# Kernel optimization log

Measured on AMD Instinct MI355X. Metric: run time of the kernel, lower is better.

## Reference

```python
import jax, jax.numpy as jnp
import numpy as np

# Dimensions
N = 16384    # batch of tree nodes (original code is batch-1 per node; math is identical per row)
WD, TD, RD = 300, 50, 50   # word / tag / rel feature dims
H = 512      # mlp_com_hid_dim
M = 512      # mem_dim == mlp_com_out_dim (required by additive gate combination)
G = 5        # gates: [i, f_down, f_left, o, u]
W_SCALE = 0.05


def setup_inputs() -> dict:
    key = jax.random.key(0)
    ks = jax.random.split(key, 32)
    def rn(i, shape, s=1.0):
        return jax.random.normal(ks[i], shape, dtype=jnp.float32) * s
    return dict(
        word=rn(0, (N, WD)), tag=rn(1, (N, TD)), rel=rn(2, (N, RD)),
        k=rn(3, (N, M)), q=rn(4, (N, M)), h_prev=rn(5, (N, M)), c_prev=rn(6, (N, M)),
        # com_MLP params, stacked over the 5 gates
        W_word=rn(7, (G, H, WD), W_SCALE), b_word=rn(8, (G, H), W_SCALE),
        W_tag=rn(9, (G, H, TD), W_SCALE),  b_tag=rn(10, (G, H), W_SCALE),
        W_rel=rn(11, (G, H, RD), W_SCALE), b_rel=rn(12, (G, H), W_SCALE),
        W_hid=rn(13, (G, H, H), W_SCALE),  b_hid=rn(14, (G, H), W_SCALE),
        W_last=rn(15, (G, M, H), W_SCALE), b_last=rn(16, (G, M), W_SCALE),
        # per-gate Linear(mem_dim, mem_dim) applied to h_prev and k
        W_hp=rn(17, (G, M, M), W_SCALE), b_hp=rn(18, (G, M), W_SCALE),
        W_k=rn(19, (G, M, M), W_SCALE),  b_k=rn(20, (G, M), W_SCALE),
    )


def reference(word, tag, rel, k, q, h_prev, c_prev,
              W_word, b_word, W_tag, b_tag, W_rel, b_rel,
              W_hid, b_hid, W_last, b_last,
              W_hp, b_hp, W_k, b_k):
    # com_MLP for all 5 gates at once (eval mode: dropout = identity)
    h0 = jnp.tanh(jnp.einsum('nw,ghw->gnh', word, W_word)
                  + jnp.einsum('nt,ght->gnh', tag, W_tag)
                  + jnp.einsum('nr,ghr->gnh', rel, W_rel)
                  + (b_word + b_tag + b_rel)[:, None, :])            # [G,N,H]
    h1 = jnp.tanh(jnp.einsum('gnh,gkh->gnk', h0, W_hid) + b_hid[:, None, :])   # hidden layer
    m = jnp.tanh(jnp.einsum('gnh,gmh->gnm', h1, W_last) + b_last[:, None, :])  # [G,N,M]
    # gate pre-activations: mlp + W_h h_prev + W_k k (with biases)
    pre = (m
           + jnp.einsum('nm,gom->gno', h_prev, W_hp) + b_hp[:, None, :]
           + jnp.einsum('nm,gom->gno', k, W_k) + b_k[:, None, :])    # [G,N,M]
    i_g    = jax.nn.sigmoid(pre[0])
    f_down = jax.nn.sigmoid(pre[1])
    f_left = jax.nn.sigmoid(pre[2])
    o_g    = jax.nn.sigmoid(pre[3])
    u_g    = jnp.tanh(pre[4])
    c = i_g * u_g + f_down * q + f_left * c_prev
    h = o_g * jnp.tanh(c)
    return (h, c)
```

## Files before the change

kernel.cpp:

```cpp
#include <hip/hip_runtime.h>
#include <math.h>

#define NROWS 16384
#define GATES 5
#define HDIM 512
#define KPAD 416

using bf16x8 = __attribute__((ext_vector_type(8))) short;
using f32x4  = __attribute__((ext_vector_type(4))) float;

__device__ inline float b2f(unsigned short s) {
  unsigned int u = ((unsigned int)s) << 16;
  return __builtin_bit_cast(float, u);
}
__device__ inline unsigned short f2b(float f) {
  unsigned int u = __builtin_bit_cast(unsigned int, f);
  u += 0x7fffu + ((u >> 16) & 1u);
  return (unsigned short)(u >> 16);
}

__device__ inline float fast_sigmoid(float x) {
  float t = __builtin_amdgcn_exp2f(-1.4426950408889634f * x);
  return __builtin_amdgcn_rcpf(1.0f + t);
}
__device__ inline float fast_tanh(float x) {
  float t = __builtin_amdgcn_exp2f(2.8853900817779268f * x);
  return 1.0f - 2.0f * __builtin_amdgcn_rcpf(1.0f + t);
}

__device__ inline void gload_lds16(const unsigned short* g, unsigned short* l) {
  __builtin_amdgcn_global_load_lds(
      (const __attribute__((address_space(1))) unsigned int*)(g),
      (__attribute__((address_space(3))) unsigned int*)(l), 16, 0, 0);
}


__global__ void pack_x(const float* __restrict__ word,
                       const float* __restrict__ tag,
                       const float* __restrict__ rel,
                       unsigned short* __restrict__ xcat) {
  int idx = blockIdx.x * 256 + threadIdx.x;
  if (idx >= NROWS * KPAD) return;
  int n = idx / KPAD, c = idx % KPAD;
  float v = 0.f;
  if (c < 300)      v = word[n * 300 + c];
  else if (c < 350) v = tag[n * 50 + (c - 300)];
  else if (c < 400) v = rel[n * 50 + (c - 350)];
  xcat[idx] = f2b(v);
}

__global__ void pack_w(const float* __restrict__ Ww,
                       const float* __restrict__ Wt,
                       const float* __restrict__ Wr,
                       unsigned short* __restrict__ Wcat) {
  int idx = blockIdx.x * 256 + threadIdx.x;
  if (idx >= GATES * HDIM * KPAD) return;
  int gh = idx / KPAD;
  int c = idx % KPAD;
  float v = 0.f;
  if (c < 300)      v = Ww[gh * 300 + c];
  else if (c < 350) v = Wt[gh * 50 + (c - 300)];
  else if (c < 400) v = Wr[gh * 50 + (c - 350)];
  Wcat[idx] = f2b(v);
}

__global__ void cvt_w4(const float* __restrict__ a, const float* __restrict__ b,
                       const float* __restrict__ c, const float* __restrict__ d,
                       unsigned short* oa, unsigned short* ob,
                       unsigned short* oc, unsigned short* od) {
  const float* in; unsigned short* out;
  switch (blockIdx.y) {
    case 0: in = a; out = oa; break;
    case 1: in = b; out = ob; break;
    case 2: in = c; out = oc; break;
    default: in = d; out = od; break;
  }
  int i = (blockIdx.x * 256 + threadIdx.x) * 4;
  float4 v = *(const float4*)(in + i);
  ushort4 o;
  o.x = f2b(v.x); o.y = f2b(v.y); o.z = f2b(v.z); o.w = f2b(v.w);
  *(ushort4*)(out + i) = o;
}

__global__ void cvt_x2(const float* __restrict__ a, const float* __restrict__ b,
                       unsigned short* oa, unsigned short* ob) {
  const float* in = blockIdx.y ? b : a;
  unsigned short* out = blockIdx.y ? ob : oa;
  int i = (blockIdx.x * 256 + threadIdx.x) * 4;
  float4 v = *(const float4*)(in + i);
  ushort4 o;
  o.x = f2b(v.x); o.y = f2b(v.y); o.z = f2b(v.z); o.w = f2b(v.w);
  *(ushort4*)(out + i) = o;
}

__global__ void pack_bias(const float* __restrict__ bw, const float* __restrict__ bt,
                          const float* __restrict__ br, const float* __restrict__ bh,
                          const float* __restrict__ bl, const float* __restrict__ bhp,
                          const float* __restrict__ bk,
                          float* bias0, float* bias1, float* bias2, float* biasD) {
  int i = blockIdx.x * 256 + threadIdx.x;
  if (i < GATES * HDIM) {
    bias0[i] = bw[i] + bt[i] + br[i];
    bias1[i] = bh[i];
    bias2[i] = bl[i];
    biasD[i] = bhp[i] + bk[i];
  }
}


template<int MODE>
__global__ __launch_bounds__(512, 2) void gemm_big(
    const unsigned short* __restrict__ A1, const unsigned short* __restrict__ A2,
    const unsigned short* __restrict__ W1, const unsigned short* __restrict__ W2,
    const float* __restrict__ bias,
    const unsigned short* __restrict__ Madd,
    unsigned short* __restrict__ Out,
    int aPerGate, int S, int ld)
{
  __shared__ __align__(16) unsigned short smem[36864];
  unsigned short* Ab0 = smem;
  unsigned short* Bb0 = smem + 24576;
  unsigned short* eps = smem;

  const int bid = (int)blockIdx.x;
  const int swz = (bid & 7) * 160 + (bid >> 3);
  const int col = swz % 20, rowt = swz / 20;
  const int row0  = rowt * 256;
  const int gcol0 = col * 128;
  const int g = gcol0 >> 9;
  const size_t aslab = aPerGate ? (size_t)g * NROWS * ld : 0;

  const int t = threadIdx.x;
  const int wid = t >> 6, l = t & 63;
  const int wrow = (wid >> 2) * 128;
  const int wcol = (wid & 3) * 32;
  const int fr = l & 15, q = l >> 4;

  f32x4 acc[8][2];
#pragma unroll
  for (int mi = 0; mi < 8; ++mi)
#pragma unroll
    for (int ni = 0; ni < 2; ++ni)
      acc[mi][ni] = (f32x4){0.f, 0.f, 0.f, 0.f};

  auto stage = [&](int c, int buf) {
    const unsigned short* Asrc; const unsigned short* Wsrc; int kloc;
    if (MODE == 1 && c >= 16) { Asrc = A2;         Wsrc = W2; kloc = (c - 16) * 32; }
    else                      { Asrc = A1 + aslab; Wsrc = W1; kloc = c * 32; }
    const int rb = t >> 2;
#pragma unroll
    for (int j = 0; j < 2; ++j) {
      const int r = j * 128 + rb;
      const int sgj = ((t & 3) ^ ((r >> 1) & 3)) * 8;
      gload_lds16(Asrc + (size_t)(row0 + r) * ld + kloc + sgj, &Ab0[buf * 8192 + j * 4096 + t * 8]);
    }
    const int sg = ((t & 3) ^ ((rb >> 1) & 3)) * 8;
    gload_lds16(Wsrc + (size_t)(gcol0 + rb) * ld + kloc + sg, &Bb0[buf * 4096 + t * 8]);
  };

  stage(0, 0);
  if (S > 1) stage(1, 1);

  for (int s = 0; s < S; ++s) {
    const int buf = s % 3;
    if (s + 2 < S) {
      stage(s + 2, (s + 2) % 3);
      asm volatile("s_waitcnt vmcnt(6)" ::: "memory");
    } else if (s + 1 < S) {
      asm volatile("s_waitcnt vmcnt(3)" ::: "memory");
    } else {
      asm volatile("s_waitcnt vmcnt(0)" ::: "memory");
    }
    __builtin_amdgcn_s_barrier();

    bf16x8 bq[2];
#pragma unroll
    for (int ni = 0; ni < 2; ++ni) {
      const int r = wcol + ni * 16 + fr;
      bq[ni] = *reinterpret_cast<const bf16x8*>(&Bb0[buf * 4096 + r * 32 + ((q ^ ((r >> 1) & 3)) * 8)]);
    }
#pragma unroll
    for (int p = 0; p < 2; ++p) {
      bf16x8 af[4];
#pragma unroll
      for (int mi = 0; mi < 4; ++mi) {
        const int r = wrow + (p * 4 + mi) * 16 + fr;
        af[mi] = *reinterpret_cast<const bf16x8*>(&Ab0[buf * 8192 + r * 32 + ((q ^ ((r >> 1) & 3)) * 8)]);
      }
      __builtin_amdgcn_s_setprio(1);
#pragma unroll
      for (int mi = 0; mi < 4; ++mi)
#pragma unroll
        for (int ni = 0; ni < 2; ++ni)
          acc[p * 4 + mi][ni] = __builtin_amdgcn_mfma_f32_16x16x32_bf16(af[mi], bq[ni], acc[p * 4 + mi][ni], 0, 0, 0);
      __builtin_amdgcn_s_setprio(0);
    }
    __builtin_amdgcn_s_barrier();
  }

  const size_t NM = (size_t)NROWS * HDIM;
  unsigned short* outg = Out + (size_t)g * NM;
  const int colbase = gcol0 & 511;
  float bv[2];
#pragma unroll
  for (int ni = 0; ni < 2; ++ni)
    bv[ni] = bias[g * HDIM + colbase + wcol + ni * 16 + fr];

#pragma unroll
  for (int h = 0; h < 4; ++h) {
    __builtin_amdgcn_s_barrier();
    if ((wid >> 2) == (h >> 1)) {
      const int mib = (h & 1) * 4;
#pragma unroll
      for (int mi2 = 0; mi2 < 4; ++mi2)
#pragma unroll
        for (int ni = 0; ni < 2; ++ni)
#pragma unroll
          for (int j = 0; j < 4; ++j)
            eps[(mi2 * 16 + q * 4 + j) * 132 + wcol + ni * 16 + fr] =
                f2b(acc[mib + mi2][ni][j] + bv[ni]);
    }
    __builtin_amdgcn_s_barrier();
#pragma unroll
    for (int v = 0; v < 2; ++v) {
      const int c  = v * 512 + t;
      const int rl = c >> 4;
      const int cc = (c & 15) * 8;
      const int gr = row0 + h * 64 + rl;
      bf16x8 pv = *reinterpret_cast<const bf16x8*>(&eps[rl * 132 + cc]);
      bf16x8 ov;
      if (MODE == 1) {
        bf16x8 mv = *reinterpret_cast<const bf16x8*>(
            Madd + (size_t)g * NM + (size_t)gr * HDIM + colbase + cc);
#pragma unroll
        for (int e = 0; e < 8; ++e) {
          float f = b2f((unsigned short)pv[e]) + b2f((unsigned short)mv[e]);
          f = (g < 4) ? fast_sigmoid(f) : fast_tanh(f);
          ov[e] = (short)f2b(f);
        }
      } else {
#pragma unroll
        for (int e = 0; e < 8; ++e)
          ov[e] = (short)f2b(fast_tanh(b2f((unsigned short)pv[e])));
      }
      *reinterpret_cast<bf16x8*>(&outg[(size_t)gr * HDIM + colbase + cc]) = ov;
    }
  }
}


__device__ inline float exb(const uint4& v, int j) {
  unsigned int wd = ((const unsigned int*)&v)[j >> 1];
  return b2f((unsigned short)(wd >> ((j & 1) * 16)));
}

__global__ void combine(const unsigned short* __restrict__ gates,
                        const float* __restrict__ q,
                        const float* __restrict__ cp,
                        float* __restrict__ out) {
  const size_t NM = (size_t)NROWS * HDIM;
  size_t i8 = ((size_t)blockIdx.x * 256 + threadIdx.x) * 8;
  if (i8 >= NM) return;
  uint4 gi = *(const uint4*)(gates + 0 * NM + i8);
  uint4 gf = *(const uint4*)(gates + 1 * NM + i8);
  uint4 gl = *(const uint4*)(gates + 2 * NM + i8);
  uint4 go = *(const uint4*)(gates + 3 * NM + i8);
  uint4 gu = *(const uint4*)(gates + 4 * NM + i8);
  float4 q0 = *(const float4*)(q + i8);
  float4 q1 = *(const float4*)(q + i8 + 4);
  float4 p0 = *(const float4*)(cp + i8);
  float4 p1 = *(const float4*)(cp + i8 + 4);
  float qv[8] = {q0.x, q0.y, q0.z, q0.w, q1.x, q1.y, q1.z, q1.w};
  float pv[8] = {p0.x, p0.y, p0.z, p0.w, p1.x, p1.y, p1.z, p1.w};
  float hv[8], cv[8];
#pragma unroll
  for (int j = 0; j < 8; ++j) {
    float c = exb(gi, j) * exb(gu, j) + exb(gf, j) * qv[j] + exb(gl, j) * pv[j];
    hv[j] = exb(go, j) * fast_tanh(c);
    cv[j] = c;
  }
  *(float4*)(out + i8)      = make_float4(hv[0], hv[1], hv[2], hv[3]);
  *(float4*)(out + i8 + 4)  = make_float4(hv[4], hv[5], hv[6], hv[7]);
  *(float4*)(out + NM + i8)     = make_float4(cv[0], cv[1], cv[2], cv[3]);
  *(float4*)(out + NM + i8 + 4) = make_float4(cv[4], cv[5], cv[6], cv[7]);
}


extern "C" void kernel_launch(void* const* d_in, const int* in_sizes, int n_in,
                              void* d_out, int out_size, void* d_ws, size_t ws_size,
                              hipStream_t stream) {
  const float* word  = (const float*)d_in[0];
  const float* tag   = (const float*)d_in[1];
  const float* rel   = (const float*)d_in[2];
  const float* kin   = (const float*)d_in[3];
  const float* qin   = (const float*)d_in[4];
  const float* hprev = (const float*)d_in[5];
  const float* cprev = (const float*)d_in[6];
  const float* Ww    = (const float*)d_in[7];
  const float* bw    = (const float*)d_in[8];
  const float* Wt    = (const float*)d_in[9];
  const float* bt    = (const float*)d_in[10];
  const float* Wr    = (const float*)d_in[11];
  const float* br    = (const float*)d_in[12];
  const float* Wh    = (const float*)d_in[13];
  const float* bh    = (const float*)d_in[14];
  const float* Wl    = (const float*)d_in[15];
  const float* bl    = (const float*)d_in[16];
  const float* Whp   = (const float*)d_in[17];
  const float* bhp   = (const float*)d_in[18];
  const float* Wk    = (const float*)d_in[19];
  const float* bk    = (const float*)d_in[20];

  char* ws = (char*)d_ws;
  unsigned short* xcat   = (unsigned short*)(ws);
  unsigned short* Wcat   = (unsigned short*)(ws + 13631488);
  unsigned short* Whb    = (unsigned short*)(ws + 15761408);
  unsigned short* Wlb    = (unsigned short*)(ws + 18382848);
  unsigned short* Whpb   = (unsigned short*)(ws + 21004288);
  unsigned short* Wkb    = (unsigned short*)(ws + 23625728);
  unsigned short* hprevb = (unsigned short*)(ws + 26247168);
  unsigned short* kb16   = (unsigned short*)(ws + 43024384);
  float* bias0           = (float*)(ws + 59801600);
  float* bias1           = (float*)(ws + 59811840);
  float* bias2           = (float*)(ws + 59822080);
  float* biasD           = (float*)(ws + 59832320);
  unsigned short* bufA   = (unsigned short*)(ws + 59842560);
  unsigned short* bufB   = (unsigned short*)(ws + 143728640);

  pack_x<<<26624, 256, 0, stream>>>(word, tag, rel, xcat);
  pack_w<<<4160, 256, 0, stream>>>(Ww, Wt, Wr, Wcat);
  cvt_w4<<<dim3(1280, 4), 256, 0, stream>>>(Wh, Wl, Whp, Wk, Whb, Wlb, Whpb, Wkb);
  cvt_x2<<<dim3(8192, 2), 256, 0, stream>>>(hprev, kin, hprevb, kb16);
  pack_bias<<<10, 256, 0, stream>>>(bw, bt, br, bh, bl, bhp, bk, bias0, bias1, bias2, biasD);

  const int grid = (NROWS / 256) * ((GATES * HDIM) / 128);
  gemm_big<0><<<grid, 512, 0, stream>>>(xcat, nullptr, Wcat, nullptr, bias0, nullptr, bufA, 0, 13, KPAD);
  gemm_big<0><<<grid, 512, 0, stream>>>(bufA, nullptr, Whb, nullptr, bias1, nullptr, bufB, 1, 16, HDIM);
  gemm_big<0><<<grid, 512, 0, stream>>>(bufB, nullptr, Wlb, nullptr, bias2, nullptr, bufA, 1, 16, HDIM);
  gemm_big<1><<<grid, 512, 0, stream>>>(hprevb, kb16, Whpb, Wkb, biasD, bufA, bufB, 0, 32, HDIM);
  combine<<<4096, 256, 0, stream>>>(bufB, qin, cprev, (float*)d_out);
}
```

Before: 391.6 us.

## Fuse last MLP layer GEMM with gate-input GEMMs into one kernel

```diff
diff --git a/kernel.cpp b/kernel.cpp
--- a/kernel.cpp
+++ b/kernel.cpp
@@ -32,6 +32,13 @@
   __builtin_amdgcn_global_load_lds(
       (const __attribute__((address_space(1))) unsigned int*)(g),
       (__attribute__((address_space(3))) unsigned int*)(l), 16, 0, 0);
+}
+
+__device__ inline void cfence() { asm volatile("" ::: "memory"); }
+__device__ inline void hard_barrier() {
+  cfence();
+  __builtin_amdgcn_s_barrier();
+  cfence();
 }
 
 
@@ -108,12 +115,11 @@
 }
 
 
-template<int MODE>
-__global__ __launch_bounds__(512, 2) void gemm_big(
-    const unsigned short* __restrict__ A1, const unsigned short* __restrict__ A2,
-    const unsigned short* __restrict__ W1, const unsigned short* __restrict__ W2,
+
+__global__ __launch_bounds__(512, 2) void gemm_mlp(
+    const unsigned short* __restrict__ A1,
+    const unsigned short* __restrict__ W1,
     const float* __restrict__ bias,
-    const unsigned short* __restrict__ Madd,
     unsigned short* __restrict__ Out,
     int aPerGate, int S, int ld)
 {
@@ -144,22 +150,22 @@
       acc[mi][ni] = (f32x4){0.f, 0.f, 0.f, 0.f};
 
   auto stage = [&](int c, int buf) {
-    const unsigned short* Asrc; const unsigned short* Wsrc; int kloc;
-    if (MODE == 1 && c >= 16) { Asrc = A2;         Wsrc = W2; kloc = (c - 16) * 32; }
-    else                      { Asrc = A1 + aslab; Wsrc = W1; kloc = c * 32; }
+    const int kloc = c * 32;
     const int rb = t >> 2;
 #pragma unroll
     for (int j = 0; j < 2; ++j) {
       const int r = j * 128 + rb;
       const int sgj = ((t & 3) ^ ((r >> 1) & 3)) * 8;
-      gload_lds16(Asrc + (size_t)(row0 + r) * ld + kloc + sgj, &Ab0[buf * 8192 + j * 4096 + t * 8]);
+      gload_lds16(A1 + aslab + (size_t)(row0 + r) * ld + kloc + sgj, &Ab0[buf * 8192 + j * 4096 + t * 8]);
     }
     const int sg = ((t & 3) ^ ((rb >> 1) & 3)) * 8;
-    gload_lds16(Wsrc + (size_t)(gcol0 + rb) * ld + kloc + sg, &Bb0[buf * 4096 + t * 8]);
+    gload_lds16(W1 + (size_t)(gcol0 + rb) * ld + kloc + sg, &Bb0[buf * 4096 + t * 8]);
   };
 
+  cfence();
   stage(0, 0);
   if (S > 1) stage(1, 1);
+  cfence();
 
   for (int s = 0; s < S; ++s) {
     const int buf = s % 3;
@@ -171,7 +177,7 @@
     } else {
       asm volatile("s_waitcnt vmcnt(0)" ::: "memory");
     }
-    __builtin_amdgcn_s_barrier();
+    hard_barrier();
 
     bf16x8 bq[2];
 #pragma unroll
@@ -195,7 +201,7 @@
           acc[p * 4 + mi][ni] = __builtin_amdgcn_mfma_f32_16x16x32_bf16(af[mi], bq[ni], acc[p * 4 + mi][ni], 0, 0, 0);
       __builtin_amdgcn_s_setprio(0);
     }
-    __builtin_amdgcn_s_barrier();
+    hard_barrier();
   }
 
   const size_t NM = (size_t)NROWS * HDIM;
@@ -208,7 +214,7 @@
 
 #pragma unroll
   for (int h = 0; h < 4; ++h) {
-    __builtin_amdgcn_s_barrier();
+    hard_barrier();
     if ((wid >> 2) == (h >> 1)) {
       const int mib = (h & 1) * 4;
 #pragma unroll
@@ -218,9 +224,10 @@
 #pragma unroll
           for (int j = 0; j < 4; ++j)
             eps[(mi2 * 16 + q * 4 + j) * 132 + wcol + ni * 16 + fr] =
-                f2b(acc[mib + mi2][ni][j] + bv[ni]);
-    }
-    __builtin_amdgcn_s_barrier();
+                f2b(fast_tanh(acc[mib + mi2][ni][j] + bv[ni]));
+    }
+    asm volatile("s_waitcnt lgkmcnt(0)" ::: "memory");
+    hard_barrier();
 #pragma unroll
     for (int v = 0; v < 2; ++v) {
       const int c  = v * 512 + t;
@@ -228,22 +235,153 @@
       const int cc = (c & 15) * 8;
       const int gr = row0 + h * 64 + rl;
       bf16x8 pv = *reinterpret_cast<const bf16x8*>(&eps[rl * 132 + cc]);
-      bf16x8 ov;
-      if (MODE == 1) {
-        bf16x8 mv = *reinterpret_cast<const bf16x8*>(
-            Madd + (size_t)g * NM + (size_t)gr * HDIM + colbase + cc);
-#pragma unroll
-        for (int e = 0; e < 8; ++e) {
-          float f = b2f((unsigned short)pv[e]) + b2f((unsigned short)mv[e]);
-          f = (g < 4) ? fast_sigmoid(f) : fast_tanh(f);
-          ov[e] = (short)f2b(f);
+      *reinterpret_cast<bf16x8*>(&outg[(size_t)gr * HDIM + colbase + cc]) = pv;
+    }
+  }
+}
+
+
+__global__ __launch_bounds__(512, 2) void gemm_cd(
+    const unsigned short* __restrict__ H1,
+    const unsigned short* __restrict__ Hp,
+    const unsigned short* __restrict__ Kb,
+    const unsigned short* __restrict__ Wl,
+    const unsigned short* __restrict__ Whp,
+    const unsigned short* __restrict__ Wk,
+    const float* __restrict__ bias2, const float* __restrict__ biasD,
+    unsigned short* __restrict__ Out)
+{
+  __shared__ __align__(16) unsigned short smem[36864];
+  unsigned short* Ab0 = smem;
+  unsigned short* Bb0 = smem + 24576;
+  unsigned short* eps = smem;
+
+  const int bid = (int)blockIdx.x;
+  const int swz = (bid & 7) * 160 + (bid >> 3);
+  const int col = swz % 20, rowt = swz / 20;
+  const int row0  = rowt * 256;
+  const int gcol0 = col * 128;
+  const int g = gcol0 >> 9;
+
+  const int t = threadIdx.x;
+  const int wid = t >> 6, l = t & 63;
+  const int wrow = (wid >> 2) * 128;
+  const int wcol = (wid & 3) * 32;
+  const int fr = l & 15, q = l >> 4;
+
+  f32x4 acc[8][2];
+#pragma unroll
+  for (int mi = 0; mi < 8; ++mi)
+#pragma unroll
+    for (int ni = 0; ni < 2; ++ni)
+      acc[mi][ni] = (f32x4){0.f, 0.f, 0.f, 0.f};
+
+  auto stageG = [&](const unsigned short* Asrc, const unsigned short* Wsrc,
+                    int kloc, int buf) {
+    const int rb = t >> 2;
+#pragma unroll
+    for (int j = 0; j < 2; ++j) {
+      const int r = j * 128 + rb;
+      const int sgj = ((t & 3) ^ ((r >> 1) & 3)) * 8;
+      gload_lds16(Asrc + (size_t)(row0 + r) * HDIM + kloc + sgj, &Ab0[buf * 8192 + j * 4096 + t * 8]);
+    }
+    const int sg = ((t & 3) ^ ((rb >> 1) & 3)) * 8;
+    gload_lds16(Wsrc + (size_t)(gcol0 + rb) * HDIM + kloc + sg, &Bb0[buf * 4096 + t * 8]);
+  };
+
+  auto runloop = [&](int S, auto srcpick) {
+    cfence();
+    { auto s0 = srcpick(0); stageG(s0.a, s0.w, s0.k, 0); }
+    if (S > 1) { auto s1 = srcpick(1); stageG(s1.a, s1.w, s1.k, 1); }
+    cfence();
+    for (int s = 0; s < S; ++s) {
+      const int buf = s % 3;
+      if (s + 2 < S) {
+        auto sn = srcpick(s + 2);
+        stageG(sn.a, sn.w, sn.k, (s + 2) % 3);
+        asm volatile("s_waitcnt vmcnt(6)" ::: "memory");
+      } else if (s + 1 < S) {
+        asm volatile("s_waitcnt vmcnt(3)" ::: "memory");
+      } else {
+        asm volatile("s_waitcnt vmcnt(0)" ::: "memory");
+      }
+      hard_barrier();
+
+      bf16x8 bq[2];
+#pragma unroll
+      for (int ni = 0; ni < 2; ++ni) {
+        const int r = wcol + ni * 16 + fr;
+        bq[ni] = *reinterpret_cast<const bf16x8*>(&Bb0[buf * 4096 + r * 32 + ((q ^ ((r >> 1) & 3)) * 8)]);
+      }
+#pragma unroll
+      for (int p = 0; p < 2; ++p) {
+        bf16x8 af[4];
+#pragma unroll
+        for (int mi = 0; mi < 4; ++mi) {
+          const int r = wrow + (p * 4 + mi) * 16 + fr;
+          af[mi] = *reinterpret_cast<const bf16x8*>(&Ab0[buf * 8192 + r * 32 + ((q ^ ((r >> 1) & 3)) * 8)]);
         }
-      } else {
-#pragma unroll
-        for (int e = 0; e < 8; ++e)
-          ov[e] = (short)f2b(fast_tanh(b2f((unsigned short)pv[e])));
+        __builtin_amdgcn_s_setprio(1);
+#pragma unroll
+        for (int mi = 0; mi < 4; ++mi)
+#pragma unroll
+          for (int ni = 0; ni < 2; ++ni)
+            acc[p * 4 + mi][ni] = __builtin_amdgcn_mfma_f32_16x16x32_bf16(af[mi], bq[ni], acc[p * 4 + mi][ni], 0, 0, 0);
+        __builtin_amdgcn_s_setprio(0);
       }
-      *reinterpret_cast<bf16x8*>(&outg[(size_t)gr * HDIM + colbase + cc]) = ov;
+      hard_barrier();
+    }
+  };
+
+  struct Src { const unsigned short* a; const unsigned short* w; int k; };
+  const size_t NM = (size_t)NROWS * HDIM;
+
+  const unsigned short* h1g = H1 + (size_t)g * NM;
+  runloop(16, [&](int c) -> Src { return {h1g, Wl, c * 32}; });
+
+  const int colbase = gcol0 & 511;
+#pragma unroll
+  for (int ni = 0; ni < 2; ++ni) {
+    const float b2 = bias2[g * HDIM + colbase + wcol + ni * 16 + fr];
+    const float bD = biasD[g * HDIM + colbase + wcol + ni * 16 + fr];
+#pragma unroll
+    for (int mi = 0; mi < 8; ++mi)
+#pragma unroll
+      for (int j = 0; j < 4; ++j)
+        acc[mi][ni][j] = fast_tanh(acc[mi][ni][j] + b2) + bD;
+  }
+
+  runloop(32, [&](int c) -> Src {
+    return (c < 16) ? Src{Hp, Whp, c * 32} : Src{Kb, Wk, (c - 16) * 32};
+  });
+
+  unsigned short* outg = Out + (size_t)g * NM;
+#pragma unroll
+  for (int h = 0; h < 4; ++h) {
+    hard_barrier();
+    if ((wid >> 2) == (h >> 1)) {
+      const int mib = (h & 1) * 4;
+#pragma unroll
+      for (int mi2 = 0; mi2 < 4; ++mi2)
+#pragma unroll
+        for (int ni = 0; ni < 2; ++ni)
+#pragma unroll
+          for (int j = 0; j < 4; ++j) {
+            float v = acc[mib + mi2][ni][j];
+            v = (g < 4) ? fast_sigmoid(v) : fast_tanh(v);
+            eps[(mi2 * 16 + q * 4 + j) * 132 + wcol + ni * 16 + fr] = f2b(v);
+          }
+    }
+    asm volatile("s_waitcnt lgkmcnt(0)" ::: "memory");
+    hard_barrier();
+#pragma unroll
+    for (int v = 0; v < 2; ++v) {
+      const int c  = v * 512 + t;
+      const int rl = c >> 4;
+      const int cc = (c & 15) * 8;
+      const int gr = row0 + h * 64 + rl;
+      bf16x8 pv = *reinterpret_cast<const bf16x8*>(&eps[rl * 132 + cc]);
+      *reinterpret_cast<bf16x8*>(&outg[(size_t)gr * HDIM + colbase + cc]) = pv;
     }
   }
 }
@@ -334,9 +472,9 @@
   pack_bias<<<10, 256, 0, stream>>>(bw, bt, br, bh, bl, bhp, bk, bias0, bias1, bias2, biasD);
 
   const int grid = (NROWS / 256) * ((GATES * HDIM) / 128);
-  gemm_big<0><<<grid, 512, 0, stream>>>(xcat, nullptr, Wcat, nullptr, bias0, nullptr, bufA, 0, 13, KPAD);
-  gemm_big<0><<<grid, 512, 0, stream>>>(bufA, nullptr, Whb, nullptr, bias1, nullptr, bufB, 1, 16, HDIM);
-  gemm_big<0><<<grid, 512, 0, stream>>>(bufB, nullptr, Wlb, nullptr, bias2, nullptr, bufA, 1, 16, HDIM);
-  gemm_big<1><<<grid, 512, 0, stream>>>(hprevb, kb16, Whpb, Wkb, biasD, bufA, bufB, 0, 32, HDIM);
-  combine<<<4096, 256, 0, stream>>>(bufB, qin, cprev, (float*)d_out);
-}
+  gemm_mlp<<<grid, 512, 0, stream>>>(xcat, Wcat, bias0, bufA, 0, 13, KPAD);
+  gemm_mlp<<<grid, 512, 0, stream>>>(bufA, Whb, bias1, bufB, 1, 16, HDIM);
+  gemm_cd<<<grid, 512, 0, stream>>>(bufB, hprevb, kb16, Wlb, Whpb, Wkb,
+                                    bias2, biasD, bufA);
+  combine<<<4096, 256, 0, stream>>>(bufA, qin, cprev, (float*)d_out);
+}
```

Result: faster. 358.7 us (-8.4%).
